# Performance work log

Hardware: AMD Instinct MI355X
Metric: run time of the kernel (lower is better)

The kernel has to match this reference:

```python
import jax, jax.numpy as jnp
import numpy as np

B, N, K = 32, 8192, 40


def _pi(x, w, b):
    # permute_invariant_layer: subtract per-(sample,feature) max over set dim,
    # then 1x1 conv1d (pointwise matmul over feature dim).
    x = x - jnp.max(x, axis=2, keepdims=True)          # [B, F, N]
    return jnp.einsum('bfn,of->bon', x, w) + b[None, :, None]


def setup_inputs() -> dict:
    key = jax.random.key(0)
    ks = jax.random.split(key, 12)
    def glorot(k, shape, fan_in):
        return jax.random.normal(k, shape, jnp.float32) * (1.0 / np.sqrt(fan_in))
    return {
        'x': jax.random.normal(ks[0], (B, 3, N), jnp.float32),
        'w1': glorot(ks[1], (64, 3), 3),   'b1': jnp.zeros((64,), jnp.float32),
        'w2': glorot(ks[2], (128, 64), 64), 'b2': jnp.zeros((128,), jnp.float32),
        'w3': glorot(ks[3], (256, 128), 128), 'b3': jnp.zeros((256,), jnp.float32),
        'fc1_w': glorot(ks[4], (128, 256), 256), 'fc1_b': jnp.zeros((128,), jnp.float32),
        'fc2_w': glorot(ks[5], (K, 128), 128),   'fc2_b': jnp.zeros((K,), jnp.float32),
    }


def reference(x, w1, b1, w2, b2, w3, b3, fc1_w, fc1_b, fc2_w, fc2_b):
    h = jnp.tanh(_pi(x, w1, b1))          # [B, 64, N]
    h = jnp.tanh(_pi(h, w2, b2))          # [B, 128, N]
    h = jnp.tanh(_pi(h, w3, b3))          # [B, 256, N]
    g = jnp.max(h, axis=2)                # global max pool -> [B, 256]
    # dropout omitted (deterministic/eval reference)
    g = jnp.tanh(g @ fc1_w.T + fc1_b)     # [B, 128]
    g = jnp.tanh(g @ fc2_w.T + fc2_b)     # [B, K]
    return jax.nn.log_softmax(g, axis=-1)
```

## Files before the change

### kernel.cpp

```cpp
#include <hip/hip_runtime.h>
#include <hip/hip_bf16.h>

#define B_  32
#define N_  8192
#define C1  64
#define C2  128
#define C3  256
#define KO  40
#define SLOTS 8

typedef __attribute__((ext_vector_type(8))) short bh8;
typedef __attribute__((ext_vector_type(4))) float f32x4;

union FragU { uint u[4]; bh8 h; uint4 v; };

#define MFMA_BF16 __builtin_amdgcn_mfma_f32_16x16x32_bf16


__device__ __forceinline__ float ftanh(float x) {
    float e = __expf(2.0f * x);
    float r = __builtin_amdgcn_rcpf(e + 1.0f);
    return fmaf(-2.0f, r, 1.0f);
}

__device__ __forceinline__ float quadMax(float v) {
    v = fmaxf(v, __shfl_xor(v, 1, 64));
    v = fmaxf(v, __shfl_xor(v, 2, 64));
    v = fmaxf(v, __shfl_xor(v, 4, 64));
    v = fmaxf(v, __shfl_xor(v, 8, 64));
    return v;
}

__device__ __forceinline__ unsigned encf(float f) {
    unsigned u = __float_as_uint(f);
    return (u & 0x80000000u) ? ~u : (u | 0x80000000u);
}
__device__ __forceinline__ float decf(unsigned e) {
    return __uint_as_float((e & 0x80000000u) ? (e & 0x7fffffffu) : ~e);
}

__device__ __forceinline__ unsigned packbf(float a, float b) {
    __hip_bfloat162 p = __float22bfloat162_rn(make_float2(a, b));
    unsigned u;
    __builtin_memcpy(&u, &p, 4);
    return u;
}


__global__ __launch_bounds__(128) void k_scan(const float* __restrict__ x,
                                              const float* __restrict__ w1,
                                              const float* __restrict__ w2,
                                              const float* __restrict__ w3,
                                              float* __restrict__ mx1p,
                                              float* __restrict__ mx2p,
                                              uint4* __restrict__ w2f,
                                              uint4* __restrict__ w3f,
                                              unsigned* __restrict__ zeroBase) {
    int t = threadIdx.x;
    int bid = blockIdx.x;
    if (bid < 256) {
        int b = bid >> 3, s = bid & 7;
        const float* xb = x + (size_t)b * 3 * N_ + s * 1024 + t;
        float x0[8], x1[8], x2[8];
#pragma unroll
        for (int i = 0; i < 8; ++i) {
            x0[i] = xb[i * 128];
            x1[i] = xb[N_ + i * 128];
            x2[i] = xb[2 * N_ + i * 128];
        }
        float c0 = x0[0], c1 = x1[0], c2 = x2[0];
#pragma unroll
        for (int i = 1; i < 8; ++i) {
            c0 = fmaxf(c0, x0[i]);
            c1 = fmaxf(c1, x1[i]);
            c2 = fmaxf(c2, x2[i]);
        }
        __shared__ float tl[67][133];
#pragma unroll
        for (int o = 0; o < C1; ++o) {
            float w0 = w1[o * 3 + 0], wa = w1[o * 3 + 1], wb = w1[o * 3 + 2];
            float m = -1e30f;
#pragma unroll
            for (int i = 0; i < 8; ++i)
                m = fmaxf(m, fmaf(x0[i], w0, fmaf(x1[i], wa, x2[i] * wb)));
            tl[o][t] = m;
        }
        tl[64][t] = c0;
        tl[65][t] = c1;
        tl[66][t] = c2;
        __syncthreads();
        if (t < 67) {
            float m = tl[t][0];
            for (int j = 1; j < 128; ++j) m = fmaxf(m, tl[t][j]);
            if (t < 64) mx2p[(s * 32 + b) * 64 + t] = m;
            else        mx1p[(s * 32 + b) * 4 + (t - 64)] = m;
        }
    } else if (bid < 296) {
        int tid = (bid - 256) * 128 + t;
        const float* src;
        uint4* dst;
        if (tid < 1024) {
            int lane = tid & 63, ks = (tid >> 6) & 1, mt = tid >> 7;
            src = w2 + (mt * 16 + (lane & 15)) * C1 + ks * 32 + (lane >> 4) * 8;
            dst = w2f + tid;
        } else {
            int fj = tid - 1024;
            int lane = fj & 63, ks = (fj >> 6) & 3, mt = fj >> 8;
            src = w3 + (mt * 16 + (lane & 15)) * C2 + ks * 32 + (lane >> 4) * 8;
            dst = w3f + fj;
        }
        uint4 o;
        o.x = packbf(src[0], src[1]);
        o.y = packbf(src[2], src[3]);
        o.z = packbf(src[4], src[5]);
        o.w = packbf(src[6], src[7]);
        *dst = o;
    } else {
        int idx = (bid - 296) * 128 + t;
        for (int i = idx; i < 8192 + 4096; i += 256) zeroBase[i] = 0u;
    }
}


__global__ __launch_bounds__(256) void k_passD(const float* __restrict__ x,
                                               const float* __restrict__ w1,
                                               const float* __restrict__ b1,
                                               const float* __restrict__ w2,
                                               const float* __restrict__ b2,
                                               const float* __restrict__ mx1p,
                                               const float* __restrict__ mx2p,
                                               const uint4* __restrict__ w2f,
                                               const uint4* __restrict__ w3f,
                                               unsigned* __restrict__ mx3e,
                                               unsigned* __restrict__ genc) {
    __shared__ uint4 h1v[8][130];
    __shared__ uint2 h2u[32][130];
    __shared__ float w1s[192];
    __shared__ float sm[3];
    __shared__ float beff1s[C1];
    __shared__ float m2s[C1];
    __shared__ float beff2s[C2];

    int b = blockIdx.x >> 6;
    int chunk = blockIdx.x & 63;
    int t = threadIdx.x;
    int p = t & 127, hh = t >> 7;
    int lane = t & 63, wv = t >> 6, qd = lane >> 4, ln = lane & 15;

    const float* xb = x + (size_t)b * 3 * N_ + chunk * 128 + p;
    float x0 = xb[0], x1 = xb[N_], x2 = xb[2 * N_];

    if (t < 192) w1s[t] = w1[t];
    float mraw = -1e30f;
    if (t < C1) {
#pragma unroll
        for (int s = 0; s < SLOTS; ++s)
            mraw = fmaxf(mraw, mx2p[(s * 32 + b) * 64 + t]);
    }
    if (t < 3) {
        float m = -1e30f;
#pragma unroll
        for (int s = 0; s < SLOTS; ++s)
            m = fmaxf(m, mx1p[(s * 32 + b) * 4 + t]);
        sm[t] = m;
    }
    __syncthreads();
    if (t < C1) {
        float be = b1[t] - sm[0] * w1s[t * 3 + 0] - sm[1] * w1s[t * 3 + 1]
                         - sm[2] * w1s[t * 3 + 2];
        beff1s[t] = be;
        m2s[t] = ftanh(mraw + be);
    }
    __syncthreads();
    if (t < C2) {
        float a = b2[t];
#pragma unroll 8
        for (int f = 0; f < C1; ++f) a -= m2s[f] * w2[t * C1 + f];
        beff2s[t] = a;
    }

#pragma unroll
    for (int qq = 0; qq < 4; ++qq) {
        int c = hh * 32 + qq * 8;
        float v[8];
#pragma unroll
        for (int s = 0; s < 8; ++s) {
            float a = beff1s[c + s];
            a = fmaf(x0, w1s[(c + s) * 3 + 0], a);
            a = fmaf(x1, w1s[(c + s) * 3 + 1], a);
            a = fmaf(x2, w1s[(c + s) * 3 + 2], a);
            v[s] = ftanh(a);
        }
        uint4 pk;
        pk.x = packbf(v[0], v[1]);
        pk.y = packbf(v[2], v[3]);
        pk.z = packbf(v[4], v[5]);
        pk.w = packbf(v[6], v[7]);
        h1v[hh * 4 + qq][p] = pk;
    }
    __syncthreads();

    {
        bh8 wf2[2][2];
        f32x4 bb2[2];
#pragma unroll
        for (int mi = 0; mi < 2; ++mi) {
            int mt = 2 * wv + mi;
#pragma unroll
            for (int ks = 0; ks < 2; ++ks) {
                FragU fu;
                fu.v = w2f[(mt * 2 + ks) * 64 + lane];
                wf2[mi][ks] = fu.h;
            }
#pragma unroll
            for (int r = 0; r < 4; ++r)
                bb2[mi][r] = beff2s[mt * 16 + qd * 4 + r];
        }
        float vmax2[2][4];
#pragma unroll
        for (int mi = 0; mi < 2; ++mi)
#pragma unroll
            for (int r = 0; r < 4; ++r) vmax2[mi][r] = -1e30f;

        for (int nb = 0; nb < 8; ++nb) {
            int n = nb * 16 + ln;
            f32x4 acc0 = bb2[0];
            f32x4 acc1 = bb2[1];
#pragma unroll
            for (int ks = 0; ks < 2; ++ks) {
                FragU fb;
                fb.v = h1v[ks * 4 + qd][n];
                acc0 = MFMA_BF16(wf2[0][ks], fb.h, acc0, 0, 0, 0);
                acc1 = MFMA_BF16(wf2[1][ks], fb.h, acc1, 0, 0, 0);
            }
#pragma unroll
            for (int mi = 0; mi < 2; ++mi) {
                f32x4 acc = mi ? acc1 : acc0;
#pragma unroll
                for (int r = 0; r < 4; ++r)
                    vmax2[mi][r] = fmaxf(vmax2[mi][r], acc[r]);
                int k4 = (2 * wv + mi) * 4 + qd;
                h2u[k4][n] = make_uint2(packbf(ftanh(acc[0]), ftanh(acc[1])),
                                        packbf(ftanh(acc[2]), ftanh(acc[3])));
            }
        }
#pragma unroll
        for (int mi = 0; mi < 2; ++mi)
#pragma unroll
            for (int r = 0; r < 4; ++r) {
                float v = quadMax(vmax2[mi][r]);
                if (ln == 0)
                    atomicMax(&mx3e[b * C2 + (2 * wv + mi) * 16 + qd * 4 + r], encf(v));
            }
    }
    __syncthreads();

    {
        bh8 wf3[4][4];
#pragma unroll
        for (int mi = 0; mi < 4; ++mi)
#pragma unroll
            for (int ks = 0; ks < 4; ++ks) {
                FragU fu;
                fu.v = w3f[((wv * 4 + mi) * 4 + ks) * 64 + lane];
                wf3[mi][ks] = fu.h;
            }
        float vmax3[4][4];
#pragma unroll
        for (int mi = 0; mi < 4; ++mi)
#pragma unroll
            for (int r = 0; r < 4; ++r) vmax3[mi][r] = -1e30f;

        for (int nb = 0; nb < 8; ++nb) {
            int n = nb * 16 + ln;
            f32x4 acc[4];
#pragma unroll
            for (int mi = 0; mi < 4; ++mi) acc[mi] = (f32x4){0.f, 0.f, 0.f, 0.f};
#pragma unroll
            for (int ks = 0; ks < 4; ++ks) {
                int kk = ks * 4 + qd;
                uint2 u0 = h2u[2 * kk][n], u1 = h2u[2 * kk + 1][n];
                FragU fb;
                fb.u[0] = u0.x; fb.u[1] = u0.y; fb.u[2] = u1.x; fb.u[3] = u1.y;
#pragma unroll
                for (int mi = 0; mi < 4; ++mi)
                    acc[mi] = MFMA_BF16(wf3[mi][ks], fb.h, acc[mi], 0, 0, 0);
            }
#pragma unroll
            for (int mi = 0; mi < 4; ++mi)
#pragma unroll
                for (int r = 0; r < 4; ++r)
                    vmax3[mi][r] = fmaxf(vmax3[mi][r], acc[mi][r]);
        }

#pragma unroll
        for (int mi = 0; mi < 4; ++mi)
#pragma unroll
            for (int r = 0; r < 4; ++r) {
                float v = quadMax(vmax3[mi][r]);
                if (ln == 0)
                    atomicMax(&genc[b * C3 + (wv * 4 + mi) * 16 + qd * 4 + r], encf(v));
            }
    }
}


__global__ __launch_bounds__(256) void k_fc(const unsigned* __restrict__ mx3e,
                                            const unsigned* __restrict__ genc,
                                            const float* __restrict__ w3,
                                            const float* __restrict__ b3,
                                            const float* __restrict__ fc1w,
                                            const float* __restrict__ fc1b,
                                            const float* __restrict__ fc2w,
                                            const float* __restrict__ fc2b,
                                            float* __restrict__ out) {
    __shared__ float m3[C2];
    __shared__ float gs[C3];
    __shared__ float hs[C2];
    __shared__ float vs[KO];
    __shared__ float red[2];
    int b = blockIdx.x, t = threadIdx.x;
    if (t < C2) m3[t] = ftanh(decf(mx3e[b * C2 + t]));
    __syncthreads();
    {
        float a = b3[t];
#pragma unroll 8
        for (int f = 0; f < C2; ++f) a -= m3[f] * w3[t * C2 + f];
        gs[t] = ftanh(decf(genc[b * C3 + t]) + a);
    }
    __syncthreads();
    if (t < C2) {
        float a = fc1b[t];
#pragma unroll 8
        for (int i = 0; i < C3; ++i) a = fmaf(gs[i], fc1w[t * C3 + i], a);
        hs[t] = ftanh(a);
    }
    __syncthreads();
    if (t < KO) {
        float a = fc2b[t];
#pragma unroll 8
        for (int i = 0; i < C2; ++i) a = fmaf(hs[i], fc2w[t * C2 + i], a);
        vs[t] = ftanh(a);
    }
    __syncthreads();
    if (t == 0) {
        float m = -1e30f;
        for (int j = 0; j < KO; ++j) m = fmaxf(m, vs[j]);
        float s = 0.0f;
        for (int j = 0; j < KO; ++j) s += __expf(vs[j] - m);
        red[0] = m;
        red[1] = __logf(s);
    }
    __syncthreads();
    if (t < KO) out[b * KO + t] = vs[t] - red[0] - red[1];
}


extern "C" void kernel_launch(void* const* d_in, const int* in_sizes, int n_in,
                              void* d_out, int out_size, void* d_ws, size_t ws_size,
                              hipStream_t stream) {
    const float* x    = (const float*)d_in[0];
    const float* w1   = (const float*)d_in[1];
    const float* b1   = (const float*)d_in[2];
    const float* w2   = (const float*)d_in[3];
    const float* b2   = (const float*)d_in[4];
    const float* w3   = (const float*)d_in[5];
    const float* b3   = (const float*)d_in[6];
    const float* fc1w = (const float*)d_in[7];
    const float* fc1b = (const float*)d_in[8];
    const float* fc2w = (const float*)d_in[9];
    const float* fc2b = (const float*)d_in[10];
    float* out = (float*)d_out;

    float* W = (float*)d_ws;
    unsigned* genc = (unsigned*)W;
    unsigned* mx3e = (unsigned*)(W + 8192);
    float*    mx1p = W + 12288;
    float*    mx2p = W + 13312;
    uint4*    w2f  = (uint4*)(W + 29696);
    uint4*    w3f  = (uint4*)(W + 33792);

    k_scan<<<298, 128, 0, stream>>>(x, w1, w2, w3, mx1p, mx2p, w2f, w3f, genc);
    k_passD<<<B_ * 64, 256, 0, stream>>>(x, w1, b1, w2, b2,
                                         mx1p, mx2p, w2f, w3f, mx3e, genc);
    k_fc<<<B_, 256, 0, stream>>>(mx3e, genc, w3, b3, fc1w, fc1b, fc2w, fc2b, out);
}
```

Before: 161.8 us.

## Use 512 threads per block in passD, splitting channel tiles across more waves

Doubles the block size of the main fused kernel to 512 threads. Each wave now owns one 16-channel tile of layer 2 and two tiles of layer 3 instead of two and four. The layer-1 work per thread is halved. This lowers per-wave register use and adds waves to hide MFMA and LDS latency. In exchange it adds more per-wave fixed overhead and more atomics, and the hidden index code (hh, p, wv) must match the new thread mapping.

```diff
diff --git a/kernel.cpp b/kernel.cpp
--- a/kernel.cpp
+++ b/kernel.cpp
@@ -122,7 +122,7 @@
 }
 
 
-__global__ __launch_bounds__(256) void k_passD(const float* __restrict__ x,
+__global__ __launch_bounds__(512) void k_passD(const float* __restrict__ x,
                                                const float* __restrict__ w1,
                                                const float* __restrict__ b1,
                                                const float* __restrict__ w2,
@@ -180,8 +180,8 @@
     }
 
 #pragma unroll
-    for (int qq = 0; qq < 4; ++qq) {
-        int c = hh * 32 + qq * 8;
+    for (int qq = 0; qq < 2; ++qq) {
+        int c = hh * 16 + qq * 8;
         float v[8];
 #pragma unroll
         for (int s = 0; s < 8; ++s) {
@@ -196,86 +196,72 @@
         pk.y = packbf(v[2], v[3]);
         pk.z = packbf(v[4], v[5]);
         pk.w = packbf(v[6], v[7]);
-        h1v[hh * 4 + qq][p] = pk;
+        h1v[hh * 2 + qq][p] = pk;
     }
     __syncthreads();
 
     {
-        bh8 wf2[2][2];
-        f32x4 bb2[2];
-#pragma unroll
-        for (int mi = 0; mi < 2; ++mi) {
-            int mt = 2 * wv + mi;
-#pragma unroll
-            for (int ks = 0; ks < 2; ++ks) {
-                FragU fu;
-                fu.v = w2f[(mt * 2 + ks) * 64 + lane];
-                wf2[mi][ks] = fu.h;
-            }
-#pragma unroll
-            for (int r = 0; r < 4; ++r)
-                bb2[mi][r] = beff2s[mt * 16 + qd * 4 + r];
-        }
-        float vmax2[2][4];
-#pragma unroll
-        for (int mi = 0; mi < 2; ++mi)
-#pragma unroll
-            for (int r = 0; r < 4; ++r) vmax2[mi][r] = -1e30f;
+        bh8 wf2[2];
+        f32x4 bb2;
+#pragma unroll
+        for (int ks = 0; ks < 2; ++ks) {
+            FragU fu;
+            fu.v = w2f[(wv * 2 + ks) * 64 + lane];
+            wf2[ks] = fu.h;
+        }
+#pragma unroll
+        for (int r = 0; r < 4; ++r)
+            bb2[r] = beff2s[wv * 16 + qd * 4 + r];
+
+        float vmax2[4];
+#pragma unroll
+        for (int r = 0; r < 4; ++r) vmax2[r] = -1e30f;
 
         for (int nb = 0; nb < 8; ++nb) {
             int n = nb * 16 + ln;
-            f32x4 acc0 = bb2[0];
-            f32x4 acc1 = bb2[1];
+            f32x4 acc = bb2;
 #pragma unroll
             for (int ks = 0; ks < 2; ++ks) {
                 FragU fb;
                 fb.v = h1v[ks * 4 + qd][n];
-                acc0 = MFMA_BF16(wf2[0][ks], fb.h, acc0, 0, 0, 0);
-                acc1 = MFMA_BF16(wf2[1][ks], fb.h, acc1, 0, 0, 0);
+                acc = MFMA_BF16(wf2[ks], fb.h, acc, 0, 0, 0);
             }
 #pragma unroll
-            for (int mi = 0; mi < 2; ++mi) {
-                f32x4 acc = mi ? acc1 : acc0;
-#pragma unroll
-                for (int r = 0; r < 4; ++r)
-                    vmax2[mi][r] = fmaxf(vmax2[mi][r], acc[r]);
-                int k4 = (2 * wv + mi) * 4 + qd;
-                h2u[k4][n] = make_uint2(packbf(ftanh(acc[0]), ftanh(acc[1])),
-                                        packbf(ftanh(acc[2]), ftanh(acc[3])));
-            }
-        }
+            for (int r = 0; r < 4; ++r)
+                vmax2[r] = fmaxf(vmax2[r], acc[r]);
+            h2u[wv * 4 + qd][n] = make_uint2(packbf(ftanh(acc[0]), ftanh(acc[1])),
+                                            packbf(ftanh(acc[2]), ftanh(acc[3])));
+        }
+#pragma unroll
+        for (int r = 0; r < 4; ++r) {
+            float v = quadMax(vmax2[r]);
+            if (ln == 0)
+                atomicMax(&mx3e[b * C2 + wv * 16 + qd * 4 + r], encf(v));
+        }
+    }
+    __syncthreads();
+
+    {
+        bh8 wf3[2][4];
 #pragma unroll
         for (int mi = 0; mi < 2; ++mi)
-#pragma unroll
-            for (int r = 0; r < 4; ++r) {
-                float v = quadMax(vmax2[mi][r]);
-                if (ln == 0)
-                    atomicMax(&mx3e[b * C2 + (2 * wv + mi) * 16 + qd * 4 + r], encf(v));
-            }
-    }
-    __syncthreads();
-
-    {
-        bh8 wf3[4][4];
-#pragma unroll
-        for (int mi = 0; mi < 4; ++mi)
 #pragma unroll
             for (int ks = 0; ks < 4; ++ks) {
                 FragU fu;
-                fu.v = w3f[((wv * 4 + mi) * 4 + ks) * 64 + lane];
+                fu.v = w3f[((2 * wv + mi) * 4 + ks) * 64 + lane];
                 wf3[mi][ks] = fu.h;
             }
-        float vmax3[4][4];
-#pragma unroll
-        for (int mi = 0; mi < 4; ++mi)
+        float vmax3[2][4];
+#pragma unroll
+        for (int mi = 0; mi < 2; ++mi)
 #pragma unroll
             for (int r = 0; r < 4; ++r) vmax3[mi][r] = -1e30f;
 
         for (int nb = 0; nb < 8; ++nb) {
             int n = nb * 16 + ln;
-            f32x4 acc[4];
-#pragma unroll
-            for (int mi = 0; mi < 4; ++mi) acc[mi] = (f32x4){0.f, 0.f, 0.f, 0.f};
+            f32x4 acc[2];
+#pragma unroll
+            for (int mi = 0; mi < 2; ++mi) acc[mi] = (f32x4){0.f, 0.f, 0.f, 0.f};
 #pragma unroll
             for (int ks = 0; ks < 4; ++ks) {
                 int kk = ks * 4 + qd;
@@ -283,23 +269,23 @@
                 FragU fb;
                 fb.u[0] = u0.x; fb.u[1] = u0.y; fb.u[2] = u1.x; fb.u[3] = u1.y;
 #pragma unroll
-                for (int mi = 0; mi < 4; ++mi)
+                for (int mi = 0; mi < 2; ++mi)
                     acc[mi] = MFMA_BF16(wf3[mi][ks], fb.h, acc[mi], 0, 0, 0);
             }
 #pragma unroll
-            for (int mi = 0; mi < 4; ++mi)
+            for (int mi = 0; mi < 2; ++mi)
 #pragma unroll
                 for (int r = 0; r < 4; ++r)
                     vmax3[mi][r] = fmaxf(vmax3[mi][r], acc[mi][r]);
         }
 
 #pragma unroll
-        for (int mi = 0; mi < 4; ++mi)
+        for (int mi = 0; mi < 2; ++mi)
 #pragma unroll
             for (int r = 0; r < 4; ++r) {
                 float v = quadMax(vmax3[mi][r]);
                 if (ln == 0)
-                    atomicMax(&genc[b * C3 + (wv * 4 + mi) * 16 + qd * 4 + r], encf(v));
+                    atomicMax(&genc[b * C3 + (2 * wv + mi) * 16 + qd * 4 + r], encf(v));
             }
     }
 }
@@ -381,7 +367,7 @@
     uint4*    w3f  = (uint4*)(W + 33792);
 
     k_scan<<<298, 128, 0, stream>>>(x, w1, w2, w3, mx1p, mx2p, w2f, w3f, genc);
-    k_passD<<<B_ * 64, 256, 0, stream>>>(x, w1, b1, w2, b2,
+    k_passD<<<B_ * 64, 512, 0, stream>>>(x, w1, b1, w2, b2,
                                          mx1p, mx2p, w2f, w3f, mx3e, genc);
     k_fc<<<B_, 256, 0, stream>>>(mx3e, genc, w3, b3, fc1w, fc1b, fc2w, fc2b, out);
 }
```

Measured after the change: 151.5 us. 6.3% less time.
